# Kernel tuning notes

Measured on AMD Instinct MI355X. Metric: run time of the kernel, lower is better.

The kernel has to match this reference:

```python
import jax, jax.numpy as jnp
import numpy as np

D_MODEL = 2048
D_INNER = 4096
D_STATE = 16
DT_RANK = 128
D_CONV = 4
EPS = 1e-5


def setup_inputs() -> dict:
    key = jax.random.key(0)
    ks = jax.random.split(key, 10)
    b, l = 1, 1024
    s = 0.02
    x = jax.random.normal(ks[0], (b, l, D_MODEL), jnp.float32)
    w_norm = jnp.ones((D_MODEL,), jnp.float32)
    W_in = jax.random.normal(ks[1], (D_MODEL, 2 * D_INNER), jnp.float32) * s
    conv_w = jax.random.normal(ks[2], (D_CONV, D_INNER), jnp.float32) * 0.3
    conv_b = jnp.zeros((D_INNER,), jnp.float32)
    W_xp = jax.random.normal(ks[3], (D_INNER, DT_RANK + 2 * D_STATE), jnp.float32) * s
    W_dt = jax.random.normal(ks[4], (DT_RANK, D_INNER), jnp.float32) * s
    b_dt = jnp.full((D_INNER,), -4.0, jnp.float32)  # softplus(-4) ~ small dt
    A_log = jnp.log(jnp.tile(jnp.arange(1, D_STATE + 1, dtype=jnp.float32), (D_INNER, 1)))
    D = jnp.ones((D_INNER,), jnp.float32)
    W_out = jax.random.normal(ks[5], (D_INNER, D_MODEL), jnp.float32) * s
    return dict(x=x, w_norm=w_norm, W_in=W_in, conv_w=conv_w, conv_b=conv_b,
                W_xp=W_xp, W_dt=W_dt, b_dt=b_dt, A_log=A_log, D=D, W_out=W_out)


def _rmsnorm(x, w):
    return x * jax.lax.rsqrt(jnp.mean(jnp.square(x), axis=-1, keepdims=True) + EPS) * w


def _depthwise_causal_conv(x, conv_w, conv_b):
    # x: (b, l, d_inner), conv_w: (d_conv, d_inner)
    k = conv_w[:, None, :]  # (W, I/groups=1, O)
    y = jax.lax.conv_general_dilated(
        x, k, window_strides=(1,), padding=((D_CONV - 1, 0),),
        dimension_numbers=('NWC', 'WIO', 'NWC'), feature_group_count=D_INNER)
    return y + conv_b


def _selective_scan(u, delta, A, B, C, D):
    # u, delta: (b,l,d); A: (d,n); B,C: (b,l,n); D: (d,)
    deltaA = jnp.exp(jnp.einsum('bld,dn->bldn', delta, A))          # (b,l,d,n)
    deltaBu = jnp.einsum('bld,bln,bld->bldn', delta, B, u)          # (b,l,d,n)
    dA = jnp.moveaxis(deltaA, 1, 0)    # (l,b,d,n)
    dBu = jnp.moveaxis(deltaBu, 1, 0)  # (l,b,d,n)
    Ct = jnp.moveaxis(C, 1, 0)         # (l,b,n)
    b, l, d = u.shape
    n = A.shape[1]

    def step(h, inputs):
        dA_t, dBu_t, C_t = inputs
        h = h * dA_t + dBu_t                       # (b,d,n)
        y = jnp.einsum('bdn,bn->bd', h, C_t)       # (b,d)
        return h, y

    h0 = jnp.zeros((b, d, n), u.dtype)
    _, ys = jax.lax.scan(step, h0, (dA, dBu, Ct))
    y = jnp.moveaxis(ys, 0, 1)                     # (b,l,d)
    return y + u * D


def reference(x, w_norm, W_in, conv_w, conv_b, W_xp, W_dt, b_dt, A_log, D, W_out):
    # ResidualBlock: out = MambaBlock(RMSNorm(x)) + x
    xn = _rmsnorm(x, w_norm)
    xz = xn @ W_in                                  # (b,l,2*d_inner)
    xs, res = jnp.split(xz, 2, axis=-1)
    xs = _depthwise_causal_conv(xs, conv_w, conv_b)
    xs = jax.nn.silu(xs)
    # SSM
    A = -jnp.exp(A_log)                             # (d_inner, n)
    xdbc = xs @ W_xp                                # (b,l,dt_rank+2n)
    dt_r = xdbc[..., :DT_RANK]
    B = xdbc[..., DT_RANK:DT_RANK + D_STATE]
    C = xdbc[..., DT_RANK + D_STATE:]
    delta = jax.nn.softplus(dt_r @ W_dt + b_dt)     # (b,l,d_inner)
    y = _selective_scan(xs, delta, A, B, C, D)
    y = y * jax.nn.silu(res)
    out = y @ W_out + x
    return out
```

## Files before the change

kernel.cpp:

```cpp
#include <hip/hip_runtime.h>
#include <math.h>

#define L_SEQ   1024
#define DMODEL  2048
#define DINNER  4096
#define DSTATE  16
#define DTRANK  128
#define N_XZ    (2 * DINNER)
#define N_XP    (DTRANK + 2 * DSTATE)
#define EPS_F   1e-5f
#define NCHUNK  32
#define TCH     32
#define SK_XP   16

using bf16x8 = __attribute__((ext_vector_type(8))) short;
using f32x4  = __attribute__((ext_vector_type(4))) float;

__device__ __forceinline__ float silu_f(float v) {
    return v * (1.0f / (1.0f + __expf(-v)));
}
__device__ __forceinline__ float softplus_f(float v) {
    return (v > 15.0f) ? v : log1pf(__expf(v));
}
__device__ __forceinline__ unsigned short f2bf(float f) {
    unsigned b = __float_as_uint(f);
    return (unsigned short)((b + 0x7FFFu + ((b >> 16) & 1u)) >> 16);
}
__device__ __forceinline__ float bf2f(unsigned short u) {
    return __uint_as_float((unsigned)u << 16);
}

#define GLOAD_LDS(gp, lp) \
    __builtin_amdgcn_global_load_lds((const __attribute__((address_space(1))) void*)(gp), \
                                     (__attribute__((address_space(3))) void*)(lp), 16, 0, 0)

__device__ __forceinline__ void transpose_body(const float* __restrict__ W,
                                               unsigned short* __restrict__ BT,
                                               int K, int N, int bx, int by,
                                               unsigned short (*Tl)[72]) {
    const int k0 = by * 64, n0 = bx * 32;
    const int kr = threadIdx.x >> 3;
    const int nc = (threadIdx.x & 7) * 4;
    float4 v0 = *(const float4*)&W[(size_t)(k0 + kr) * N + n0 + nc];
    float4 v1 = *(const float4*)&W[(size_t)(k0 + kr + 32) * N + n0 + nc];
    Tl[nc + 0][kr] = f2bf(v0.x); Tl[nc + 1][kr] = f2bf(v0.y);
    Tl[nc + 2][kr] = f2bf(v0.z); Tl[nc + 3][kr] = f2bf(v0.w);
    Tl[nc + 0][kr + 32] = f2bf(v1.x); Tl[nc + 1][kr + 32] = f2bf(v1.y);
    Tl[nc + 2][kr + 32] = f2bf(v1.z); Tl[nc + 3][kr + 32] = f2bf(v1.w);
    __syncthreads();
    const int n = threadIdx.x >> 3;
    const int k8 = (threadIdx.x & 7) * 8;
    *(bf16x8*)&BT[(size_t)(n0 + n) * K + k0 + k8] = *(const bf16x8*)&Tl[n][k8];
}

__global__ __launch_bounds__(256) void prep_kernel(const float* __restrict__ W_in,
                                                   const float* __restrict__ W_xp,
                                                   const float* __restrict__ W_dt,
                                                   const float* __restrict__ W_out,
                                                   const float* __restrict__ x,
                                                   const float* __restrict__ wn,
                                                   unsigned short* __restrict__ BT_in,
                                                   unsigned short* __restrict__ BTxp,
                                                   unsigned short* __restrict__ BTdt,
                                                   unsigned short* __restrict__ BT_out,
                                                   unsigned short* __restrict__ xn_bf) {
    __shared__ unsigned short Tl[32][72];
    __shared__ float red[4];
    int b = blockIdx.x;
    if (b < 8192) {
        transpose_body(W_in, BT_in, DMODEL, N_XZ, b % 256, b / 256, Tl);
    } else if (b < 12288) {
        b -= 8192;
        transpose_body(W_out, BT_out, DINNER, DMODEL, b % 64, b / 64, Tl);
    } else if (b < 12608) {
        b -= 12288;
        transpose_body(W_xp, BTxp, DINNER, N_XP, b % 5, b / 5, Tl);
    } else if (b < 12864) {
        b -= 12608;
        transpose_body(W_dt, BTdt, DTRANK, DINNER, b % 128, b / 128, Tl);
    } else {
        const int row = b - 12864;
        const float4* xr = (const float4*)(x + (size_t)row * DMODEL);
        float ss = 0.f;
        float4 v0 = xr[threadIdx.x];
        float4 v1 = xr[threadIdx.x + 256];
        ss += v0.x*v0.x + v0.y*v0.y + v0.z*v0.z + v0.w*v0.w;
        ss += v1.x*v1.x + v1.y*v1.y + v1.z*v1.z + v1.w*v1.w;
        #pragma unroll
        for (int o = 32; o > 0; o >>= 1) ss += __shfl_down(ss, o);
        const int lane = threadIdx.x & 63, wv = threadIdx.x >> 6;
        if (lane == 0) red[wv] = ss;
        __syncthreads();
        if (threadIdx.x == 0) {
            float t = red[0] + red[1] + red[2] + red[3];
            red[0] = rsqrtf(t / (float)DMODEL + EPS_F);
        }
        __syncthreads();
        const float scale = red[0];
        const float4* wr = (const float4*)wn;
        float4 w0 = wr[threadIdx.x];
        float4 w1 = wr[threadIdx.x + 256];
        ushort4 o0, o1;
        o0.x = f2bf(v0.x * scale * w0.x); o0.y = f2bf(v0.y * scale * w0.y);
        o0.z = f2bf(v0.z * scale * w0.z); o0.w = f2bf(v0.w * scale * w0.w);
        o1.x = f2bf(v1.x * scale * w1.x); o1.y = f2bf(v1.y * scale * w1.y);
        o1.z = f2bf(v1.z * scale * w1.z); o1.w = f2bf(v1.w * scale * w1.w);
        unsigned short* outr = xn_bf + (size_t)row * DMODEL;
        *(ushort4*)&outr[threadIdx.x * 4] = o0;
        *(ushort4*)&outr[1024 + threadIdx.x * 4] = o1;
    }
}

template <int BM, int BN, int KC, int OUTM>
__global__ __launch_bounds__(256) void gemm_mfma_kernel(const unsigned short* __restrict__ A,
                                                        const unsigned short* __restrict__ BT,
                                                        void* __restrict__ Cv,
                                                        int K, int Kc, int ldc, int Ncols,
                                                        const float* __restrict__ aux) {
    constexpr int MT = BM / 32;
    constexpr int NT = BN / 32;
    __shared__ __align__(16) unsigned short Al[KC * BM * 32];
    __shared__ __align__(16) unsigned short Bl[KC * BN * 32];
    const int tid = threadIdx.x;
    const int lane = tid & 63, wave = tid >> 6;
    const int wm = wave >> 1, wn = wave & 1;
    const int bm = blockIdx.y * BM, bn = blockIdx.x * BN;
    const size_t koff = (size_t)blockIdx.z * Kc;
    float* Cf = (float*)Cv;
    if (OUTM == 2) Cf += (size_t)blockIdx.z * (size_t)gridDim.y * BM * ldc;
    const int sr = lane >> 2;
    const int sk = (((lane & 3) ^ ((sr >> 1) & 3))) * 8;
    const int fr = lane & 15;
    const int fq = lane >> 4;
    const int fsw = (fq ^ ((fr >> 1) & 3)) * 8;

    f32x4 acc[MT][NT];
    #pragma unroll
    for (int i = 0; i < MT; ++i)
        #pragma unroll
        for (int j = 0; j < NT; ++j)
            acc[i][j] = (f32x4){0.f, 0.f, 0.f, 0.f};

    for (int k0 = 0; k0 < Kc; k0 += 32 * KC) {
        #pragma unroll
        for (int p = 0; p < KC; ++p) {
            #pragma unroll
            for (int is = wave; is < BM / 16; is += 4)
                GLOAD_LDS(&A[(size_t)(bm + is * 16 + sr) * K + koff + k0 + p * 32 + sk],
                          &Al[p * BM * 32 + is * 512]);
            #pragma unroll
            for (int is = wave; is < BN / 16; is += 4)
                GLOAD_LDS(&BT[(size_t)(bn + is * 16 + sr) * K + koff + k0 + p * 32 + sk],
                          &Bl[p * BN * 32 + is * 512]);
        }
        __syncthreads();
        #pragma unroll
        for (int p = 0; p < KC; ++p) {
            bf16x8 af[MT], bfr[NT];
            #pragma unroll
            for (int i = 0; i < MT; ++i)
                af[i] = *(const bf16x8*)&Al[p * BM * 32 + (wm * (BM / 2) + i * 16 + fr) * 32 + fsw];
            #pragma unroll
            for (int j = 0; j < NT; ++j)
                bfr[j] = *(const bf16x8*)&Bl[p * BN * 32 + (wn * (BN / 2) + j * 16 + fr) * 32 + fsw];
            #pragma unroll
            for (int i = 0; i < MT; ++i)
                #pragma unroll
                for (int j = 0; j < NT; ++j)
                    acc[i][j] = __builtin_amdgcn_mfma_f32_16x16x32_bf16(af[i], bfr[j], acc[i][j], 0, 0, 0);
        }
        __syncthreads();
    }

    #pragma unroll
    for (int i = 0; i < MT; ++i) {
        const int row = bm + wm * (BM / 2) + i * 16 + fq * 4;
        #pragma unroll
        for (int j = 0; j < NT; ++j) {
            const int col = bn + wn * (BN / 2) + j * 16 + fr;
            if (col < Ncols) {
                #pragma unroll
                for (int r = 0; r < 4; ++r) {
                    float v = acc[i][j][r];
                    if (OUTM == 0) {
                        ((unsigned short*)Cv)[(size_t)(row + r) * ldc + col] = f2bf(v);
                    } else if (OUTM == 1) {
                        ((unsigned short*)Cv)[(size_t)(row + r) * ldc + col] =
                            f2bf(softplus_f(v + aux[col]));
                    } else if (OUTM == 2) {
                        Cf[(size_t)(row + r) * ldc + col] = v;
                    } else {
                        Cf[(size_t)(row + r) * ldc + col] =
                            v + aux[(size_t)(row + r) * ldc + col];
                    }
                }
            }
        }
    }
}

__global__ __launch_bounds__(256) void conv_silu_kernel(const unsigned short* __restrict__ xz_bf,
                                                        const float* __restrict__ cw,
                                                        const float* __restrict__ cb,
                                                        unsigned short* __restrict__ xs_bf) {
    const int idx = blockIdx.x * 256 + threadIdx.x;
    const int t = idx >> 12;
    const int c = idx & (DINNER - 1);
    float acc = cb[c];
    #pragma unroll
    for (int k = 0; k < 4; ++k) {
        const int tt = t + k - 3;
        if (tt >= 0) acc = fmaf(bf2f(xz_bf[(size_t)tt * N_XZ + c]), cw[k * DINNER + c], acc);
    }
    xs_bf[idx] = f2bf(silu_f(acc));
}

__global__ __launch_bounds__(256) void reduce_sk_kernel(const float* __restrict__ part,
                                                        float* __restrict__ xdbc,
                                                        unsigned short* __restrict__ xdbc_dt) {
    const int i = blockIdx.x * 256 + threadIdx.x;
    float s = 0.f;
    #pragma unroll
    for (int c = 0; c < SK_XP; ++c) s += part[(size_t)c * (L_SEQ * N_XP) + i];
    xdbc[i] = s;
    const int col = i % N_XP;
    if (col < DTRANK) xdbc_dt[(i / N_XP) * DTRANK + col] = f2bf(s);
}

__global__ __launch_bounds__(256) void scan_pass1(const unsigned short* __restrict__ delta_bf,
                                                  const unsigned short* __restrict__ xs_bf,
                                                  const float* __restrict__ xdbc,
                                                  const float* __restrict__ A_log,
                                                  float* __restrict__ S,
                                                  float* __restrict__ sumdl) {
    __shared__ float BC[TCH][32];
    const int c = blockIdx.y;
    const int d = blockIdx.x * 256 + threadIdx.x;
    const int t0 = c * TCH;
    {
        const int tt = threadIdx.x >> 3, q = threadIdx.x & 7;
        *(float4*)&BC[tt][q * 4] =
            *(const float4*)&xdbc[(size_t)(t0 + tt) * N_XP + DTRANK + q * 4];
    }
    __syncthreads();
    float Aa[16];
    #pragma unroll
    for (int n = 0; n < 16; ++n) Aa[n] = -__expf(A_log[d * 16 + n]);
    float h[16];
    #pragma unroll
    for (int n = 0; n < 16; ++n) h[n] = 0.f;
    float sd = 0.f;
    for (int t = 0; t < TCH; ++t) {
        const float dl = bf2f(delta_bf[(size_t)(t0 + t) * DINNER + d]);
        const float u  = bf2f(xs_bf[(size_t)(t0 + t) * DINNER + d]);
        sd += dl;
        const float du = dl * u;
        #pragma unroll
        for (int n = 0; n < 16; ++n)
            h[n] = fmaf(h[n], __expf(dl * Aa[n]), du * BC[t][n]);
    }
    float* Sp = &S[((size_t)c * DINNER + d) * 16];
    #pragma unroll
    for (int n = 0; n < 16; n += 4)
        *(float4*)&Sp[n] = make_float4(h[n], h[n + 1], h[n + 2], h[n + 3]);
    sumdl[c * DINNER + d] = sd;
}

__global__ __launch_bounds__(256) void scan_pass2(const float* __restrict__ S,
                                                  const float* __restrict__ sumdl,
                                                  const float* __restrict__ A_log,
                                                  float* __restrict__ h0) {
    const int i = blockIdx.x * 256 + threadIdx.x;
    const int dd = i >> 4;
    const float A = -__expf(A_log[i]);
    float h = 0.f;
    #pragma unroll
    for (int c = 0; c < NCHUNK; ++c) {
        h0[(size_t)c * (DINNER * 16) + i] = h;
        h = h * __expf(A * sumdl[c * DINNER + dd]) + S[(size_t)c * (DINNER * 16) + i];
    }
}

__global__ __launch_bounds__(256) void scan_pass3(const unsigned short* __restrict__ delta_bf,
                                                  const unsigned short* __restrict__ xs_bf,
                                                  const float* __restrict__ xdbc,
                                                  const unsigned short* __restrict__ xz_bf,
                                                  const float* __restrict__ A_log,
                                                  const float* __restrict__ Dp,
                                                  const float* __restrict__ h0,
                                                  unsigned short* __restrict__ yg_bf) {
    __shared__ float BC[TCH][32];
    const int c = blockIdx.y;
    const int d = blockIdx.x * 256 + threadIdx.x;
    const int t0 = c * TCH;
    {
        const int tt = threadIdx.x >> 3, q = threadIdx.x & 7;
        *(float4*)&BC[tt][q * 4] =
            *(const float4*)&xdbc[(size_t)(t0 + tt) * N_XP + DTRANK + q * 4];
    }
    __syncthreads();
    float Aa[16];
    #pragma unroll
    for (int n = 0; n < 16; ++n) Aa[n] = -__expf(A_log[d * 16 + n]);
    float h[16];
    const float* h0p = &h0[(size_t)c * (DINNER * 16) + d * 16];
    #pragma unroll
    for (int n = 0; n < 16; n += 4) {
        float4 v = *(const float4*)&h0p[n];
        h[n] = v.x; h[n + 1] = v.y; h[n + 2] = v.z; h[n + 3] = v.w;
    }
    const float Dd = Dp[d];
    for (int t = 0; t < TCH; ++t) {
        const float dl = bf2f(delta_bf[(size_t)(t0 + t) * DINNER + d]);
        const float u  = bf2f(xs_bf[(size_t)(t0 + t) * DINNER + d]);
        const float du = dl * u;
        float y = 0.f;
        #pragma unroll
        for (int n = 0; n < 16; ++n) {
            h[n] = fmaf(h[n], __expf(dl * Aa[n]), du * BC[t][n]);
            y = fmaf(h[n], BC[t][16 + n], y);
        }
        const float res = bf2f(xz_bf[(size_t)(t0 + t) * N_XZ + DINNER + d]);
        yg_bf[(size_t)(t0 + t) * DINNER + d] = f2bf((y + u * Dd) * silu_f(res));
    }
}

extern "C" void kernel_launch(void* const* d_in, const int* in_sizes, int n_in,
                              void* d_out, int out_size, void* d_ws, size_t ws_size,
                              hipStream_t stream) {
    const float* x     = (const float*)d_in[0];
    const float* wn    = (const float*)d_in[1];
    const float* W_in  = (const float*)d_in[2];
    const float* cw    = (const float*)d_in[3];
    const float* cb    = (const float*)d_in[4];
    const float* W_xp  = (const float*)d_in[5];
    const float* W_dt  = (const float*)d_in[6];
    const float* b_dt  = (const float*)d_in[7];
    const float* A_log = (const float*)d_in[8];
    const float* Dp    = (const float*)d_in[9];
    const float* W_out = (const float*)d_in[10];
    float* out = (float*)d_out;

    float* ws = (float*)d_ws;
    unsigned short* xz_bf    = (unsigned short*)ws;
    unsigned short* xs_bf    = (unsigned short*)(ws + 4194304);
    unsigned short* yg_bf    = (unsigned short*)(ws + 6291456);
    unsigned short* delta_bf = (unsigned short*)(ws + 8388608);
    float*          part     = ws + 10485760;
    float*          S        = ws + 13107200;
    float*          sumdl    = ws + 15204352;
    float*          h0       = ws + 15335424;
    float*          xdbc     = ws + 17432576;
    unsigned short* xn_bf    = (unsigned short*)(ws + 17596416);
    unsigned short* BTxp     = (unsigned short*)(ws + 18644992);
    unsigned short* BTdt     = (unsigned short*)(ws + 18972672);
    unsigned short* xdbc_dt  = (unsigned short*)(ws + 19234816);
    unsigned short* BT_in    = (unsigned short*)(ws + 19300352);
    unsigned short* BT_out   = (unsigned short*)(ws + 27688960);

    prep_kernel<<<13888, 256, 0, stream>>>(W_in, W_xp, W_dt, W_out, x, wn,
                                           BT_in, BTxp, BTdt, BT_out, xn_bf);
    gemm_mfma_kernel<64, 128, 2, 0><<<dim3(N_XZ / 128, L_SEQ / 64), 256, 0, stream>>>(
        xn_bf, BT_in, xz_bf, DMODEL, DMODEL, N_XZ, N_XZ, nullptr);
    conv_silu_kernel<<<(L_SEQ * DINNER) / 256, 256, 0, stream>>>(xz_bf, cw, cb, xs_bf);
    gemm_mfma_kernel<64, 64, 2, 2><<<dim3(3, L_SEQ / 64, SK_XP), 256, 0, stream>>>(
        xs_bf, BTxp, part, DINNER, DINNER / SK_XP, N_XP, N_XP, nullptr);
    reduce_sk_kernel<<<(L_SEQ * N_XP) / 256, 256, 0, stream>>>(part, xdbc, xdbc_dt);
    gemm_mfma_kernel<64, 64, 2, 1><<<dim3(DINNER / 64, L_SEQ / 64), 256, 0, stream>>>(
        xdbc_dt, BTdt, delta_bf, DTRANK, DTRANK, DINNER, DINNER, b_dt);
    scan_pass1<<<dim3(DINNER / 256, NCHUNK), 256, 0, stream>>>(delta_bf, xs_bf, xdbc, A_log, S, sumdl);
    scan_pass2<<<(DINNER * 16) / 256, 256, 0, stream>>>(S, sumdl, A_log, h0);
    scan_pass3<<<dim3(DINNER / 256, NCHUNK), 256, 0, stream>>>(delta_bf, xs_bf, xdbc, xz_bf,
                                                               A_log, Dp, h0, yg_bf);
    gemm_mfma_kernel<64, 64, 2, 3><<<dim3(DMODEL / 64, L_SEQ / 64), 256, 0, stream>>>(
        yg_bf, BT_out, out, DINNER, DINNER, DMODEL, DMODEL, x);
}
```

Measured before the change: 336.9 us.

## Fuse post-in-projection stages into persistent kernel with grid barriers

```diff
diff --git a/kernel.cpp b/kernel.cpp
--- a/kernel.cpp
+++ b/kernel.cpp
@@ -12,6 +12,7 @@
 #define NCHUNK  32
 #define TCH     32
 #define SK_XP   16
+#define MGRID   512
 
 using bf16x8 = __attribute__((ext_vector_type(8))) short;
 using f32x4  = __attribute__((ext_vector_type(4))) float;
@@ -33,6 +34,18 @@
 #define GLOAD_LDS(gp, lp) \
     __builtin_amdgcn_global_load_lds((const __attribute__((address_space(1))) void*)(gp), \
                                      (__attribute__((address_space(3))) void*)(lp), 16, 0, 0)
+
+__device__ __forceinline__ void gbar(unsigned* cnt, int idx, unsigned total) {
+    __syncthreads();
+    if (threadIdx.x == 0) {
+        __threadfence();
+        atomicAdd(&cnt[idx], 1u);
+        while (__hip_atomic_load(&cnt[idx], __ATOMIC_RELAXED, __HIP_MEMORY_SCOPE_AGENT) < total)
+            __builtin_amdgcn_s_sleep(16);
+        __threadfence();
+    }
+    __syncthreads();
+}
 
 __device__ __forceinline__ void transpose_body(const float* __restrict__ W,
                                                unsigned short* __restrict__ BT,
@@ -63,10 +76,12 @@
                                                    unsigned short* __restrict__ BTxp,
                                                    unsigned short* __restrict__ BTdt,
                                                    unsigned short* __restrict__ BT_out,
-                                                   unsigned short* __restrict__ xn_bf) {
+                                                   unsigned short* __restrict__ xn_bf,
+                                                   unsigned* __restrict__ barcnt) {
     __shared__ unsigned short Tl[32][72];
     __shared__ float red[4];
     int b = blockIdx.x;
+    if (b == 0 && threadIdx.x < 16) barcnt[threadIdx.x] = 0;
     if (b < 8192) {
         transpose_body(W_in, BT_in, DMODEL, N_XZ, b % 256, b / 256, Tl);
     } else if (b < 12288) {
@@ -111,12 +126,11 @@
     }
 }
 
-template <int BM, int BN, int KC, int OUTM>
+template <int BM, int BN, int KC>
 __global__ __launch_bounds__(256) void gemm_mfma_kernel(const unsigned short* __restrict__ A,
                                                         const unsigned short* __restrict__ BT,
-                                                        void* __restrict__ Cv,
-                                                        int K, int Kc, int ldc, int Ncols,
-                                                        const float* __restrict__ aux) {
+                                                        unsigned short* __restrict__ C,
+                                                        int K, int ldc) {
     constexpr int MT = BM / 32;
     constexpr int NT = BN / 32;
     __shared__ __align__(16) unsigned short Al[KC * BM * 32];
@@ -125,9 +139,6 @@
     const int lane = tid & 63, wave = tid >> 6;
     const int wm = wave >> 1, wn = wave & 1;
     const int bm = blockIdx.y * BM, bn = blockIdx.x * BN;
-    const size_t koff = (size_t)blockIdx.z * Kc;
-    float* Cf = (float*)Cv;
-    if (OUTM == 2) Cf += (size_t)blockIdx.z * (size_t)gridDim.y * BM * ldc;
     const int sr = lane >> 2;
     const int sk = (((lane & 3) ^ ((sr >> 1) & 3))) * 8;
     const int fr = lane & 15;
@@ -141,16 +152,16 @@
         for (int j = 0; j < NT; ++j)
             acc[i][j] = (f32x4){0.f, 0.f, 0.f, 0.f};
 
-    for (int k0 = 0; k0 < Kc; k0 += 32 * KC) {
+    for (int k0 = 0; k0 < K; k0 += 32 * KC) {
         #pragma unroll
         for (int p = 0; p < KC; ++p) {
             #pragma unroll
             for (int is = wave; is < BM / 16; is += 4)
-                GLOAD_LDS(&A[(size_t)(bm + is * 16 + sr) * K + koff + k0 + p * 32 + sk],
+                GLOAD_LDS(&A[(size_t)(bm + is * 16 + sr) * K + k0 + p * 32 + sk],
                           &Al[p * BM * 32 + is * 512]);
             #pragma unroll
             for (int is = wave; is < BN / 16; is += 4)
-                GLOAD_LDS(&BT[(size_t)(bn + is * 16 + sr) * K + koff + k0 + p * 32 + sk],
+                GLOAD_LDS(&BT[(size_t)(bn + is * 16 + sr) * K + k0 + p * 32 + sk],
                           &Bl[p * BN * 32 + is * 512]);
         }
         __syncthreads();
@@ -178,19 +189,75 @@
         #pragma unroll
         for (int j = 0; j < NT; ++j) {
             const int col = bn + wn * (BN / 2) + j * 16 + fr;
+            #pragma unroll
+            for (int r = 0; r < 4; ++r)
+                C[(size_t)(row + r) * ldc + col] = f2bf(acc[i][j][r]);
+        }
+    }
+}
+
+template <int OUTM>
+__device__ __forceinline__ void gemm_tile64(const unsigned short* A,
+                                            const unsigned short* BT,
+                                            void* Cv,
+                                            int K, int Kc, int koff,
+                                            int ldc, int Ncols,
+                                            int bm, int bn,
+                                            const float* aux,
+                                            unsigned short (&Al)[2048],
+                                            unsigned short (&Bl)[2048]) {
+    const int tid = threadIdx.x;
+    const int lane = tid & 63, wave = tid >> 6;
+    const int wm = wave >> 1, wn = wave & 1;
+    const int sr = lane >> 2;
+    const int sk = (((lane & 3) ^ ((sr >> 1) & 3))) * 8;
+    const int fr = lane & 15;
+    const int fq = lane >> 4;
+    const int fsw = (fq ^ ((fr >> 1) & 3)) * 8;
+
+    f32x4 acc[2][2];
+    #pragma unroll
+    for (int i = 0; i < 2; ++i)
+        #pragma unroll
+        for (int j = 0; j < 2; ++j)
+            acc[i][j] = (f32x4){0.f, 0.f, 0.f, 0.f};
+
+    for (int k0 = 0; k0 < Kc; k0 += 32) {
+        GLOAD_LDS(&A[(size_t)(bm + wave * 16 + sr) * K + koff + k0 + sk], &Al[wave * 512]);
+        GLOAD_LDS(&BT[(size_t)(bn + wave * 16 + sr) * K + koff + k0 + sk], &Bl[wave * 512]);
+        __syncthreads();
+        bf16x8 af[2], bfr[2];
+        #pragma unroll
+        for (int i = 0; i < 2; ++i)
+            af[i] = *(const bf16x8*)&Al[(wm * 32 + i * 16 + fr) * 32 + fsw];
+        #pragma unroll
+        for (int j = 0; j < 2; ++j)
+            bfr[j] = *(const bf16x8*)&Bl[(wn * 32 + j * 16 + fr) * 32 + fsw];
+        #pragma unroll
+        for (int i = 0; i < 2; ++i)
+            #pragma unroll
+            for (int j = 0; j < 2; ++j)
+                acc[i][j] = __builtin_amdgcn_mfma_f32_16x16x32_bf16(af[i], bfr[j], acc[i][j], 0, 0, 0);
+        __syncthreads();
+    }
+
+    #pragma unroll
+    for (int i = 0; i < 2; ++i) {
+        const int row = bm + wm * 32 + i * 16 + fq * 4;
+        #pragma unroll
+        for (int j = 0; j < 2; ++j) {
+            const int col = bn + wn * 32 + j * 16 + fr;
             if (col < Ncols) {
                 #pragma unroll
                 for (int r = 0; r < 4; ++r) {
                     float v = acc[i][j][r];
-                    if (OUTM == 0) {
-                        ((unsigned short*)Cv)[(size_t)(row + r) * ldc + col] = f2bf(v);
-                    } else if (OUTM == 1) {
+                    if (OUTM == 1) {
                         ((unsigned short*)Cv)[(size_t)(row + r) * ldc + col] =
                             f2bf(softplus_f(v + aux[col]));
                     } else if (OUTM == 2) {
-                        Cf[(size_t)(row + r) * ldc + col] = v;
+                        ((float*)Cv)[(size_t)(row + r) * ldc + col] = v;
                     } else {
-                        Cf[(size_t)(row + r) * ldc + col] =
+                        ((float*)Cv)[(size_t)(row + r) * ldc + col] =
                             v + aux[(size_t)(row + r) * ldc + col];
                     }
                 }
@@ -199,47 +266,18 @@
     }
 }
 
-__global__ __launch_bounds__(256) void conv_silu_kernel(const unsigned short* __restrict__ xz_bf,
-                                                        const float* __restrict__ cw,
-                                                        const float* __restrict__ cb,
-                                                        unsigned short* __restrict__ xs_bf) {
-    const int idx = blockIdx.x * 256 + threadIdx.x;
-    const int t = idx >> 12;
-    const int c = idx & (DINNER - 1);
-    float acc = cb[c];
-    #pragma unroll
-    for (int k = 0; k < 4; ++k) {
-        const int tt = t + k - 3;
-        if (tt >= 0) acc = fmaf(bf2f(xz_bf[(size_t)tt * N_XZ + c]), cw[k * DINNER + c], acc);
-    }
-    xs_bf[idx] = f2bf(silu_f(acc));
-}
-
-__global__ __launch_bounds__(256) void reduce_sk_kernel(const float* __restrict__ part,
-                                                        float* __restrict__ xdbc,
-                                                        unsigned short* __restrict__ xdbc_dt) {
-    const int i = blockIdx.x * 256 + threadIdx.x;
-    float s = 0.f;
-    #pragma unroll
-    for (int c = 0; c < SK_XP; ++c) s += part[(size_t)c * (L_SEQ * N_XP) + i];
-    xdbc[i] = s;
-    const int col = i % N_XP;
-    if (col < DTRANK) xdbc_dt[(i / N_XP) * DTRANK + col] = f2bf(s);
-}
-
-__global__ __launch_bounds__(256) void scan_pass1(const unsigned short* __restrict__ delta_bf,
-                                                  const unsigned short* __restrict__ xs_bf,
-                                                  const float* __restrict__ xdbc,
-                                                  const float* __restrict__ A_log,
-                                                  float* __restrict__ S,
-                                                  float* __restrict__ sumdl) {
-    __shared__ float BC[TCH][32];
-    const int c = blockIdx.y;
-    const int d = blockIdx.x * 256 + threadIdx.x;
+__device__ __forceinline__ void scan1_body(int dblk, int c,
+                                           const unsigned short* delta_bf,
+                                           const unsigned short* xs_bf,
+                                           const float* xdbc,
+                                           const float* A_log,
+                                           float* S, float* sumdl,
+                                           float (&BCs)[TCH][32]) {
+    const int d = dblk * 256 + threadIdx.x;
     const int t0 = c * TCH;
     {
         const int tt = threadIdx.x >> 3, q = threadIdx.x & 7;
-        *(float4*)&BC[tt][q * 4] =
+        *(float4*)&BCs[tt][q * 4] =
             *(const float4*)&xdbc[(size_t)(t0 + tt) * N_XP + DTRANK + q * 4];
     }
     __syncthreads();
@@ -257,45 +295,31 @@
         const float du = dl * u;
         #pragma unroll
         for (int n = 0; n < 16; ++n)
-            h[n] = fmaf(h[n], __expf(dl * Aa[n]), du * BC[t][n]);
+            h[n] = fmaf(h[n], __expf(dl * Aa[n]), du * BCs[t][n]);
     }
     float* Sp = &S[((size_t)c * DINNER + d) * 16];
     #pragma unroll
     for (int n = 0; n < 16; n += 4)
         *(float4*)&Sp[n] = make_float4(h[n], h[n + 1], h[n + 2], h[n + 3]);
     sumdl[c * DINNER + d] = sd;
-}
-
-__global__ __launch_bounds__(256) void scan_pass2(const float* __restrict__ S,
-                                                  const float* __restrict__ sumdl,
-                                                  const float* __restrict__ A_log,
-                                                  float* __restrict__ h0) {
-    const int i = blockIdx.x * 256 + threadIdx.x;
-    const int dd = i >> 4;
-    const float A = -__expf(A_log[i]);
-    float h = 0.f;
-    #pragma unroll
-    for (int c = 0; c < NCHUNK; ++c) {
-        h0[(size_t)c * (DINNER * 16) + i] = h;
-        h = h * __expf(A * sumdl[c * DINNER + dd]) + S[(size_t)c * (DINNER * 16) + i];
-    }
-}
-
-__global__ __launch_bounds__(256) void scan_pass3(const unsigned short* __restrict__ delta_bf,
-                                                  const unsigned short* __restrict__ xs_bf,
-                                                  const float* __restrict__ xdbc,
-                                                  const unsigned short* __restrict__ xz_bf,
-                                                  const float* __restrict__ A_log,
-                                                  const float* __restrict__ Dp,
-                                                  const float* __restrict__ h0,
-                                                  unsigned short* __restrict__ yg_bf) {
-    __shared__ float BC[TCH][32];
-    const int c = blockIdx.y;
-    const int d = blockIdx.x * 256 + threadIdx.x;
+    __syncthreads();
+}
+
+__device__ __forceinline__ void scan3_body(int dblk, int c,
+                                           const unsigned short* delta_bf,
+                                           const unsigned short* xs_bf,
+                                           const float* xdbc,
+                                           const unsigned short* xz_bf,
+                                           const float* A_log,
+                                           const float* Dp,
+                                           const float* h0,
+                                           unsigned short* yg_bf,
+                                           float (&BCs)[TCH][32]) {
+    const int d = dblk * 256 + threadIdx.x;
     const int t0 = c * TCH;
     {
         const int tt = threadIdx.x >> 3, q = threadIdx.x & 7;
-        *(float4*)&BC[tt][q * 4] =
+        *(float4*)&BCs[tt][q * 4] =
             *(const float4*)&xdbc[(size_t)(t0 + tt) * N_XP + DTRANK + q * 4];
     }
     __syncthreads();
@@ -317,11 +341,103 @@
         float y = 0.f;
         #pragma unroll
         for (int n = 0; n < 16; ++n) {
-            h[n] = fmaf(h[n], __expf(dl * Aa[n]), du * BC[t][n]);
-            y = fmaf(h[n], BC[t][16 + n], y);
+            h[n] = fmaf(h[n], __expf(dl * Aa[n]), du * BCs[t][n]);
+            y = fmaf(h[n], BCs[t][16 + n], y);
         }
         const float res = bf2f(xz_bf[(size_t)(t0 + t) * N_XZ + DINNER + d]);
         yg_bf[(size_t)(t0 + t) * DINNER + d] = f2bf((y + u * Dd) * silu_f(res));
+    }
+    __syncthreads();
+}
+
+__global__ __launch_bounds__(256, 2) void mega_kernel(
+    const unsigned short* __restrict__ xz_bf, const float* __restrict__ cw,
+    const float* __restrict__ cb, unsigned short* __restrict__ xs_bf,
+    const unsigned short* __restrict__ BTxp, float* __restrict__ part,
+    float* __restrict__ xdbc, unsigned short* __restrict__ xdbc_dt,
+    const unsigned short* __restrict__ BTdt, const float* __restrict__ b_dt,
+    unsigned short* __restrict__ delta_bf,
+    const float* __restrict__ A_log, const float* __restrict__ Dp,
+    float* __restrict__ S, float* __restrict__ sumdl, float* __restrict__ h0,
+    unsigned short* __restrict__ yg_bf,
+    const unsigned short* __restrict__ BT_out, const float* __restrict__ x,
+    float* __restrict__ out, unsigned* __restrict__ barcnt) {
+    __shared__ __align__(16) unsigned short Al[2048];
+    __shared__ __align__(16) unsigned short Bl[2048];
+    __shared__ float BCs[TCH][32];
+    const int bid = blockIdx.x;
+    const int tid = threadIdx.x;
+
+    for (int idx = bid * 256 + tid; idx < L_SEQ * DINNER; idx += MGRID * 256) {
+        const int t = idx >> 12;
+        const int c = idx & (DINNER - 1);
+        float acc = cb[c];
+        #pragma unroll
+        for (int k = 0; k < 4; ++k) {
+            const int tt = t + k - 3;
+            if (tt >= 0) acc = fmaf(bf2f(xz_bf[(size_t)tt * N_XZ + c]), cw[k * DINNER + c], acc);
+        }
+        xs_bf[idx] = f2bf(silu_f(acc));
+    }
+    gbar(barcnt, 0, MGRID);
+
+    for (int tb = bid; tb < 3 * 16 * SK_XP; tb += MGRID) {
+        const int bx = tb % 3, by = (tb / 3) & 15, bz = tb / 48;
+        gemm_tile64<2>(xs_bf, BTxp, part + (size_t)bz * (L_SEQ * N_XP),
+                       DINNER, DINNER / SK_XP, bz * (DINNER / SK_XP),
+                       N_XP, N_XP, by * 64, bx * 64, nullptr, Al, Bl);
+    }
+    gbar(barcnt, 1, MGRID);
+
+    for (int i = bid * 256 + tid; i < L_SEQ * N_XP; i += MGRID * 256) {
+        float s = 0.f;
+        #pragma unroll
+        for (int z = 0; z < SK_XP; ++z) s += part[(size_t)z * (L_SEQ * N_XP) + i];
+        xdbc[i] = s;
+        const int col = i % N_XP;
+        if (col < DTRANK) xdbc_dt[(i / N_XP) * DTRANK + col] = f2bf(s);
+    }
+    gbar(barcnt, 2, MGRID);
+
+    for (int tb = bid; tb < 64 * 16; tb += MGRID) {
+        const int bx = tb & 63, by = tb >> 6;
+        gemm_tile64<1>(xdbc_dt, BTdt, delta_bf, DTRANK, DTRANK, 0,
+                       DINNER, DINNER, by * 64, bx * 64, b_dt, Al, Bl);
+    }
+    gbar(barcnt, 3, MGRID);
+
+    {
+        const int tb = bid;
+        scan1_body(tb & 15, tb >> 4, delta_bf, xs_bf, xdbc, A_log, S, sumdl, BCs);
+    }
+    gbar(barcnt, 4, MGRID);
+
+    {
+        const int i = bid * 256 + tid;
+        if (i < DINNER * DSTATE) {
+            const int dd = i >> 4;
+            const float A = -__expf(A_log[i]);
+            float h = 0.f;
+            #pragma unroll
+            for (int c = 0; c < NCHUNK; ++c) {
+                h0[(size_t)c * (DINNER * 16) + i] = h;
+                h = h * __expf(A * sumdl[c * DINNER + dd]) + S[(size_t)c * (DINNER * 16) + i];
+            }
+        }
+    }
+    gbar(barcnt, 5, MGRID);
+
+    {
+        const int tb = bid;
+        scan3_body(tb & 15, tb >> 4, delta_bf, xs_bf, xdbc, xz_bf,
+                   A_log, Dp, h0, yg_bf, BCs);
+    }
+    gbar(barcnt, 6, MGRID);
+
+    {
+        const int bx = bid & 31, by = bid >> 5;
+        gemm_tile64<3>(yg_bf, BT_out, out, DINNER, DINNER, 0,
+                       DMODEL, DMODEL, by * 64, bx * 64, x, Al, Bl);
     }
 }
 
@@ -357,21 +473,16 @@
     unsigned short* xdbc_dt  = (unsigned short*)(ws + 19234816);
     unsigned short* BT_in    = (unsigned short*)(ws + 19300352);
     unsigned short* BT_out   = (unsigned short*)(ws + 27688960);
+    unsigned*       barcnt   = (unsigned*)(ws + 31883264);
 
     prep_kernel<<<13888, 256, 0, stream>>>(W_in, W_xp, W_dt, W_out, x, wn,
-                                           BT_in, BTxp, BTdt, BT_out, xn_bf);
-    gemm_mfma_kernel<64, 128, 2, 0><<<dim3(N_XZ / 128, L_SEQ / 64), 256, 0, stream>>>(
-        xn_bf, BT_in, xz_bf, DMODEL, DMODEL, N_XZ, N_XZ, nullptr);
-    conv_silu_kernel<<<(L_SEQ * DINNER) / 256, 256, 0, stream>>>(xz_bf, cw, cb, xs_bf);
-    gemm_mfma_kernel<64, 64, 2, 2><<<dim3(3, L_SEQ / 64, SK_XP), 256, 0, stream>>>(
-        xs_bf, BTxp, part, DINNER, DINNER / SK_XP, N_XP, N_XP, nullptr);
-    reduce_sk_kernel<<<(L_SEQ * N_XP) / 256, 256, 0, stream>>>(part, xdbc, xdbc_dt);
-    gemm_mfma_kernel<64, 64, 2, 1><<<dim3(DINNER / 64, L_SEQ / 64), 256, 0, stream>>>(
-        xdbc_dt, BTdt, delta_bf, DTRANK, DTRANK, DINNER, DINNER, b_dt);
-    scan_pass1<<<dim3(DINNER / 256, NCHUNK), 256, 0, stream>>>(delta_bf, xs_bf, xdbc, A_log, S, sumdl);
-    scan_pass2<<<(DINNER * 16) / 256, 256, 0, stream>>>(S, sumdl, A_log, h0);
-    scan_pass3<<<dim3(DINNER / 256, NCHUNK), 256, 0, stream>>>(delta_bf, xs_bf, xdbc, xz_bf,
-                                                               A_log, Dp, h0, yg_bf);
-    gemm_mfma_kernel<64, 64, 2, 3><<<dim3(DMODEL / 64, L_SEQ / 64), 256, 0, stream>>>(
-        yg_bf, BT_out, out, DINNER, DINNER, DMODEL, DMODEL, x);
-}
+                                           BT_in, BTxp, BTdt, BT_out, xn_bf, barcnt);
+    gemm_mfma_kernel<64, 128, 2><<<dim3(N_XZ / 128, L_SEQ / 64), 256, 0, stream>>>(
+        xn_bf, BT_in, xz_bf, DMODEL, N_XZ);
+    mega_kernel<<<MGRID, 256, 0, stream>>>(
+        xz_bf, cw, cb, xs_bf,
+        BTxp, part, xdbc, xdbc_dt,
+        BTdt, b_dt, delta_bf,
+        A_log, Dp, S, sumdl, h0, yg_bf,
+        BT_out, x, out, barcnt);
+}
```

After: 727.4 us. +115.9%, slower.
